# Kernel optimization log

Hardware: AMD Instinct MI355X
Metric: run time of the kernel (lower is better)

Reference implementation:

```python
import jax, jax.numpy as jnp
import numpy as np

N = 16384            # number of input vectors
CODEBOOK_SIZE = 8192  # M
DIM = 256             # dim_feature
BETA = 0.25           # commitment_weight


def setup_inputs() -> dict:
    key = jax.random.key(0)
    kx, ke = jax.random.split(key)
    x = jax.random.normal(kx, (N, DIM), dtype=jnp.float32)
    # kaiming-uniform-style init for the codebook
    bound = float(np.sqrt(3.0 / DIM))
    embeddings = jax.random.uniform(ke, (CODEBOOK_SIZE, DIM), dtype=jnp.float32,
                                    minval=-bound, maxval=bound)
    return {"x": x, "embeddings": embeddings}


def reference(x, embeddings):
    # l2_dist: sqrt(sum((x_i - e_j)^2)) computed via the GEMM expansion
    x2 = jnp.sum(x * x, axis=1, keepdims=True)               # (N, 1)
    e2 = jnp.sum(embeddings * embeddings, axis=1)            # (M,)
    d2 = x2 + e2[None, :] - 2.0 * (x @ embeddings.T)         # (N, M)
    dist = jnp.sqrt(jnp.maximum(d2, 0.0))
    # deterministic gumbel_sample path (training eval / stochastic=False):
    # argmax of logits = -dist  <=>  argmin of dist
    ind = jnp.argmin(dist, axis=1)                           # (N,)
    quantized = embeddings[ind]                              # one_hot @ embeddings
    # commitment loss: beta * ||x_q - sg(x)||^2 (docstring)
    commit_loss = BETA * jnp.mean((quantized - jax.lax.stop_gradient(x)) ** 2)
    # straight-through estimator
    quantized_st = x + jax.lax.stop_gradient(quantized - x)
    # perplexity from per-code counts (one-hot scatter)
    counts = jnp.zeros((CODEBOOK_SIZE,), jnp.float32).at[ind].add(1.0)
    probs = counts / counts.sum()
    perplexity = jnp.exp(-jnp.sum(probs * jnp.log(probs + 1e-10)))
    return quantized_st, ind, commit_loss, perplexity
```

## Files before the change

### kernel.cpp

```cpp
#include <hip/hip_runtime.h>
#include <stdint.h>


#define N_VEC 16384
#define M_CODES 8192
#define DIM 256
#define BETA 0.25f

#define NSLICE 8
#define SLICE_CODES 1024
#define BM 128
#define BN 128
#define BK 32
#define NPART 16
#define LDS_HALF 32768

typedef __attribute__((ext_vector_type(4))) float f32x4;
typedef __attribute__((ext_vector_type(8))) __bf16 bf16x8;

__device__ __forceinline__ void gll16(const void* g, const void* lds) {
    __builtin_amdgcn_global_load_lds(
        (const __attribute__((address_space(1))) uint32_t*)(uintptr_t)g,
        (__attribute__((address_space(3))) uint32_t*)(uint32_t)(uintptr_t)lds,
        16, 0, 0);
}

#define PIPE_SYNC() do { \
    asm volatile("s_waitcnt vmcnt(0)" ::: "memory"); \
    asm volatile("s_barrier" ::: "memory"); \
} while (0)

__device__ __forceinline__ ushort f2bf(float f) {
    uint32_t u = __float_as_uint(f);
    return (ushort)((u + 0x7FFFu + ((u >> 16) & 1u)) >> 16);
}
__device__ __forceinline__ float bf2f(ushort h) {
    return __uint_as_float(((uint32_t)h) << 16);
}

__global__ __launch_bounds__(256) void prep_kernel(
    const float* __restrict__ x, const float* __restrict__ emb,
    ushort* __restrict__ xh, ushort* __restrict__ xl,
    ushort* __restrict__ eh, ushort* __restrict__ el,
    float* __restrict__ e2) {
    const int wave = threadIdx.x >> 6;
    const int lane = threadIdx.x & 63;
    const int row = blockIdx.x * 4 + wave;

    const float* src;
    ushort* ph;
    ushort* pl;
    bool is_e;
    int er = row - N_VEC;
    if (row < N_VEC) {
        src = x + (size_t)row * DIM;
        ph = xh + (size_t)row * DIM;
        pl = xl + (size_t)row * DIM;
        is_e = false;
    } else {
        src = emb + (size_t)er * DIM;
        ph = eh + (size_t)er * DIM;
        pl = el + (size_t)er * DIM;
        is_e = true;
    }
    float4 v = *(const float4*)(src + lane * 4);
    ushort h0 = f2bf(v.x), h1 = f2bf(v.y), h2 = f2bf(v.z), h3 = f2bf(v.w);
    ushort l0 = f2bf(v.x - bf2f(h0)), l1 = f2bf(v.y - bf2f(h1));
    ushort l2 = f2bf(v.z - bf2f(h2)), l3 = f2bf(v.w - bf2f(h3));
    *(ushort4*)(ph + lane * 4) = make_ushort4(h0, h1, h2, h3);
    *(ushort4*)(pl + lane * 4) = make_ushort4(l0, l1, l2, l3);
    if (is_e) {
        float s = v.x * v.x + v.y * v.y + v.z * v.z + v.w * v.w;
        #pragma unroll
        for (int off = 32; off; off >>= 1) s += __shfl_xor(s, off);
        if (lane == 0) e2[er] = s;
    }
}

__global__ __launch_bounds__(256, 2) void vq_mfma_kernel(
    const ushort* __restrict__ xh, const ushort* __restrict__ xl,
    const ushort* __restrict__ eh, const ushort* __restrict__ el,
    const float* __restrict__ e2g, unsigned long long* __restrict__ partials) {
    extern __shared__ char lds[];

    const int t = threadIdx.x;
    const int lane = t & 63;
    const int wv = t >> 6;
    const int lane15 = lane & 15;
    const int l16 = lane >> 4;

    const int bid = blockIdx.x;
    const int rt = bid & 127;
    const int slice = bid >> 7;
    const int row0 = rt * BM;
    const int cslice0 = slice * SLICE_CODES;

    const int wr0 = (wv & 1) * 64;
    const int wc0 = (wv >> 1) * 64;

    int byteA[4], byteB[4];
    #pragma unroll
    for (int f = 0; f < 4; ++f) {
        int ra = wr0 + f * 16 + lane15;
        byteA[f] = ra * 64 + (((l16 ^ (ra >> 1)) & 3) << 4);
        int rb = wc0 + f * 16 + lane15;
        byteB[f] = rb * 64 + (((l16 ^ (rb >> 1)) & 3) << 4);
    }

    const int s0 = wv * 128 + lane;
    const int s1 = s0 + 64;
    const int r0s = s0 >> 2, r1s = s1 >> 2;
    const int c0s = ((s0 & 3) ^ ((s0 >> 3) & 3)) << 3;
    const int c1s = ((s1 & 3) ^ ((s1 >> 3) & 3)) << 3;
    const ushort* pxh0 = xh + (size_t)(row0 + r0s) * DIM + c0s;
    const ushort* pxh1 = xh + (size_t)(row0 + r1s) * DIM + c1s;
    const ushort* pxl0 = xl + (size_t)(row0 + r0s) * DIM + c0s;
    const ushort* pxl1 = xl + (size_t)(row0 + r1s) * DIM + c1s;
    const ushort* peh0 = eh + (size_t)(cslice0 + r0s) * DIM + c0s;
    const ushort* peh1 = eh + (size_t)(cslice0 + r1s) * DIM + c1s;
    const ushort* pel0 = el + (size_t)(cslice0 + r0s) * DIM + c0s;
    const ushort* pel1 = el + (size_t)(cslice0 + r1s) * DIM + c1s;

    float best[16];
    int bidx[16];
    #pragma unroll
    for (int s = 0; s < 16; ++s) { best[s] = __uint_as_float(0x7f800000u); bidx[s] = 0; }

    f32x4 acc[4][4];
    #pragma unroll
    for (int fi = 0; fi < 4; ++fi)
        #pragma unroll
        for (int fj = 0; fj < 4; ++fj) acc[fi][fj] = (f32x4){0.f, 0.f, 0.f, 0.f};

    auto stage = [&](int buf, int ks) {
        const int ct = ks >> 3;
        const int kc = ks & 7;
        const size_t xo = (size_t)(kc << 5);
        const size_t eo = (size_t)ct * ((size_t)BN * DIM) + (kc << 5);
        char* l0 = lds + buf * LDS_HALF + wv * 2048;
        char* l1 = l0 + 1024;
        gll16(pxh0 + xo, l0);
        gll16(pxh1 + xo, l1);
        gll16(pxl0 + xo, l0 + 8192);
        gll16(pxl1 + xo, l1 + 8192);
        gll16(peh0 + eo, l0 + 16384);
        gll16(peh1 + eo, l1 + 16384);
        gll16(pel0 + eo, l0 + 24576);
        gll16(pel1 + eo, l1 + 24576);
    };

    stage(0, 0);
    PIPE_SYNC();

    int cur = 0;
    for (int ks = 0; ks < 64; ++ks) {
        if (ks < 63) stage(cur ^ 1, ks + 1);

        const char* lb = lds + cur * LDS_HALF;
        bf16x8 ah[4], bh[4];
        #pragma unroll
        for (int f = 0; f < 4; ++f) {
            ah[f] = *(const bf16x8*)(lb + byteA[f]);
            bh[f] = *(const bf16x8*)(lb + 16384 + byteB[f]);
        }
        #pragma unroll
        for (int fi = 0; fi < 4; ++fi)
            #pragma unroll
            for (int fj = 0; fj < 4; ++fj)
                acc[fi][fj] = __builtin_amdgcn_mfma_f32_16x16x32_bf16(
                    ah[fi], bh[fj], acc[fi][fj], 0, 0, 0);
        bf16x8 blo[4];
        #pragma unroll
        for (int f = 0; f < 4; ++f) blo[f] = *(const bf16x8*)(lb + 24576 + byteB[f]);
        #pragma unroll
        for (int fi = 0; fi < 4; ++fi)
            #pragma unroll
            for (int fj = 0; fj < 4; ++fj)
                acc[fi][fj] = __builtin_amdgcn_mfma_f32_16x16x32_bf16(
                    ah[fi], blo[fj], acc[fi][fj], 0, 0, 0);
        bf16x8 alo[4];
        #pragma unroll
        for (int f = 0; f < 4; ++f) alo[f] = *(const bf16x8*)(lb + 8192 + byteA[f]);
        #pragma unroll
        for (int fi = 0; fi < 4; ++fi)
            #pragma unroll
            for (int fj = 0; fj < 4; ++fj)
                acc[fi][fj] = __builtin_amdgcn_mfma_f32_16x16x32_bf16(
                    alo[fi], bh[fj], acc[fi][fj], 0, 0, 0);

        PIPE_SYNC();
        cur ^= 1;

        if ((ks & 7) == 7) {
            const int cb = cslice0 + (ks >> 3) * BN + wc0;
            #pragma unroll
            for (int fj = 0; fj < 4; ++fj) {
                const int c = cb + fj * 16 + lane15;
                const float e2v = e2g[c];
                #pragma unroll
                for (int fi = 0; fi < 4; ++fi)
                    #pragma unroll
                    for (int r = 0; r < 4; ++r) {
                        float sc = e2v - 2.0f * acc[fi][fj][r];
                        const int slot = fi * 4 + r;
                        if (sc < best[slot]) { best[slot] = sc; bidx[slot] = c; }
                    }
            }
            #pragma unroll
            for (int fi = 0; fi < 4; ++fi)
                #pragma unroll
                for (int fj = 0; fj < 4; ++fj) acc[fi][fj] = (f32x4){0.f, 0.f, 0.f, 0.f};
        }
    }

    #pragma unroll
    for (int slot = 0; slot < 16; ++slot) {
        float v = best[slot];
        int ix = bidx[slot];
        #pragma unroll
        for (int off = 1; off < 16; off <<= 1) {
            float v2 = __shfl_xor(v, off);
            int ix2 = __shfl_xor(ix, off);
            if (v2 < v || (v2 == v && ix2 < ix)) { v = v2; ix = ix2; }
        }
        if (lane15 == 0) {
            int fi = slot >> 2, r = slot & 3;
            int row = row0 + wr0 + fi * 16 + l16 * 4 + r;
            uint32_t u = __float_as_uint(v);
            uint32_t ord = (u & 0x80000000u) ? ~u : (u | 0x80000000u);
            partials[(size_t)(slice * 2 + (wv >> 1)) * N_VEC + row] =
                ((unsigned long long)ord << 32) | (unsigned)ix;
        }
    }
}

__global__ __launch_bounds__(256) void finish_kernel(
    const float* __restrict__ x, const float* __restrict__ emb,
    const unsigned long long* __restrict__ partials,
    float* __restrict__ out_ind, float* __restrict__ out_q,
    unsigned* __restrict__ counts, float* __restrict__ loss_acc) {
    __shared__ float partial[4];
    const int wave = threadIdx.x >> 6;
    const int lane = threadIdx.x & 63;
    const int row = blockIdx.x * 4 + wave;

    unsigned long long m = ~0ull;
    if (lane < NPART) m = partials[(size_t)lane * N_VEC + row];
    #pragma unroll
    for (int off = 1; off < NPART; off <<= 1) {
        unsigned long long v = __shfl_xor(m, off);
        if (v < m) m = v;
    }
    m = __shfl(m, 0);
    const int ix = (int)(unsigned)(m & 0xFFFFFFFFull);

    float4 q = *(const float4*)(emb + (size_t)ix * DIM + lane * 4);
    float4 xv = *(const float4*)(x + (size_t)row * DIM + lane * 4);
    *(float4*)(out_q + (size_t)row * DIM + lane * 4) = q;
    float dx = q.x - xv.x, dy = q.y - xv.y, dz = q.z - xv.z, dw = q.w - xv.w;
    float s = dx * dx + dy * dy + dz * dz + dw * dw;
    #pragma unroll
    for (int off = 32; off; off >>= 1) s += __shfl_xor(s, off);
    if (lane == 0) {
        out_ind[row] = (float)ix;
        atomicAdd(&counts[ix], 1u);
        partial[wave] = s;
    }
    __syncthreads();
    if (threadIdx.x == 0)
        atomicAdd(loss_acc, partial[0] + partial[1] + partial[2] + partial[3]);
}

__global__ __launch_bounds__(256) void finalize_kernel(
    const unsigned* __restrict__ counts, const float* __restrict__ loss_acc,
    float* __restrict__ out_scalars) {
    __shared__ float red[256];
    float h = 0.0f;
    for (int c = threadIdx.x; c < M_CODES; c += 256) {
        float p = (float)counts[c] * (1.0f / (float)N_VEC);
        h += p * logf(p + 1e-10f);
    }
    red[threadIdx.x] = h;
    __syncthreads();
    for (int s = 128; s; s >>= 1) {
        if (threadIdx.x < s) red[threadIdx.x] += red[threadIdx.x + s];
        __syncthreads();
    }
    if (threadIdx.x == 0) {
        out_scalars[0] = BETA * loss_acc[0] / (float)(N_VEC * DIM);
        out_scalars[1] = expf(-red[0]);
    }
}

extern "C" void kernel_launch(void* const* d_in, const int* in_sizes, int n_in,
                              void* d_out, int out_size, void* d_ws, size_t ws_size,
                              hipStream_t stream) {
    const float* x = (const float*)d_in[0];
    const float* emb = (const float*)d_in[1];

    float* out = (float*)d_out;
    float* out_q = out;
    float* out_ind = out + (size_t)N_VEC * DIM;
    float* out_scalars = out_ind + N_VEC;

    ushort* xh = (ushort*)out;
    ushort* xl = xh + (size_t)N_VEC * DIM;

    char* wp = (char*)d_ws;
    ushort* eh = (ushort*)wp;  wp += (size_t)M_CODES * DIM * 2;
    ushort* el = (ushort*)wp;  wp += (size_t)M_CODES * DIM * 2;
    float* e2 = (float*)wp;    wp += (size_t)M_CODES * 4;
    unsigned long long* partials = (unsigned long long*)wp;
    wp += (size_t)NPART * N_VEC * 8;
    unsigned* counts = (unsigned*)wp; wp += (size_t)M_CODES * 4;
    float* loss_acc = (float*)wp;

    hipMemsetAsync(counts, 0, M_CODES * 4, stream);
    hipMemsetAsync(loss_acc, 0, 4, stream);

    prep_kernel<<<(N_VEC + M_CODES) / 4, 256, 0, stream>>>(x, emb, xh, xl, eh, el, e2);

    hipFuncSetAttribute((const void*)vq_mfma_kernel,
                        hipFuncAttributeMaxDynamicSharedMemorySize, 2 * LDS_HALF);
    vq_mfma_kernel<<<128 * NSLICE, 256, 2 * LDS_HALF, stream>>>(xh, xl, eh, el, e2,
                                                                partials);

    finish_kernel<<<N_VEC / 4, 256, 0, stream>>>(x, emb, partials, out_ind, out_q,
                                                 counts, loss_acc);
    finalize_kernel<<<1, 256, 0, stream>>>(counts, loss_acc, out_scalars);
}
```

Measured before the change: 277.2 us.

## Use 256-row tiles with 512 threads and a three-stage global-to-LDS ring

Doubles the row tile to 256 per block, run by 8 waves, so each staged codebook tile is shared by more rows. The double buffer with a full vmcnt(0) wait becomes a three-slot LDS ring that prefetches two steps ahead and waits only on the oldest step's loads. It also caches the slice's e2 values in LDS, raises wave priority around the MFMA bursts, reorders block indices so the slice varies fastest, and moves the counts/loss zeroing into prep_kernel to drop the memsets. The roughly 148 KB of LDS per block limits each CU to one block, and the larger tile adds register pressure.

```diff
diff --git a/kernel.cpp b/kernel.cpp
--- a/kernel.cpp
+++ b/kernel.cpp
@@ -9,26 +9,24 @@
 
 #define NSLICE 8
 #define SLICE_CODES 1024
-#define BM 128
+#define BM 256
 #define BN 128
 #define BK 32
 #define NPART 16
-#define LDS_HALF 32768
+#define STEP_BYTES 49152
+#define RING_BYTES (3 * STEP_BYTES)
+#define LDS_TOTAL (RING_BYTES + 4096)
+#define NSTEPS 64
 
 typedef __attribute__((ext_vector_type(4))) float f32x4;
 typedef __attribute__((ext_vector_type(8))) __bf16 bf16x8;
 
-__device__ __forceinline__ void gll16(const void* g, const void* lds) {
+__device__ __forceinline__ void gll16(const void* g, const void* lds_p) {
     __builtin_amdgcn_global_load_lds(
         (const __attribute__((address_space(1))) uint32_t*)(uintptr_t)g,
-        (__attribute__((address_space(3))) uint32_t*)(uint32_t)(uintptr_t)lds,
+        (__attribute__((address_space(3))) uint32_t*)(uint32_t)(uintptr_t)lds_p,
         16, 0, 0);
 }
-
-#define PIPE_SYNC() do { \
-    asm volatile("s_waitcnt vmcnt(0)" ::: "memory"); \
-    asm volatile("s_barrier" ::: "memory"); \
-} while (0)
 
 __device__ __forceinline__ ushort f2bf(float f) {
     uint32_t u = __float_as_uint(f);
@@ -42,7 +40,13 @@
     const float* __restrict__ x, const float* __restrict__ emb,
     ushort* __restrict__ xh, ushort* __restrict__ xl,
     ushort* __restrict__ eh, ushort* __restrict__ el,
-    float* __restrict__ e2) {
+    float* __restrict__ e2, unsigned* __restrict__ counts,
+    float* __restrict__ loss_acc) {
+    if (blockIdx.x < 8) {
+        int4 z = {0, 0, 0, 0};
+        ((int4*)counts)[blockIdx.x * 256 + threadIdx.x] = z;
+        if (blockIdx.x == 0 && threadIdx.x == 0) *loss_acc = 0.0f;
+    }
     const int wave = threadIdx.x >> 6;
     const int lane = threadIdx.x & 63;
     const int row = blockIdx.x * 4 + wave;
@@ -77,7 +81,7 @@
     }
 }
 
-__global__ __launch_bounds__(256, 2) void vq_mfma_kernel(
+__global__ __launch_bounds__(512, 2) void vq_mfma_kernel(
     const ushort* __restrict__ xh, const ushort* __restrict__ xl,
     const ushort* __restrict__ eh, const ushort* __restrict__ el,
     const float* __restrict__ e2g, unsigned long long* __restrict__ partials) {
@@ -89,14 +93,13 @@
     const int lane15 = lane & 15;
     const int l16 = lane >> 4;
 
-    const int bid = blockIdx.x;
-    const int rt = bid & 127;
-    const int slice = bid >> 7;
+    const int slice = blockIdx.x & 7;
+    const int rt = blockIdx.x >> 3;
     const int row0 = rt * BM;
     const int cslice0 = slice * SLICE_CODES;
 
-    const int wr0 = (wv & 1) * 64;
-    const int wc0 = (wv >> 1) * 64;
+    const int wr0 = (wv & 3) * 64;
+    const int wc0 = (wv >> 2) * 64;
 
     int byteA[4], byteB[4];
     #pragma unroll
@@ -107,19 +110,19 @@
         byteB[f] = rb * 64 + (((l16 ^ (rb >> 1)) & 3) << 4);
     }
 
-    const int s0 = wv * 128 + lane;
-    const int s1 = s0 + 64;
-    const int r0s = s0 >> 2, r1s = s1 >> 2;
-    const int c0s = ((s0 & 3) ^ ((s0 >> 3) & 3)) << 3;
-    const int c1s = ((s1 & 3) ^ ((s1 >> 3) & 3)) << 3;
-    const ushort* pxh0 = xh + (size_t)(row0 + r0s) * DIM + c0s;
-    const ushort* pxh1 = xh + (size_t)(row0 + r1s) * DIM + c1s;
-    const ushort* pxl0 = xl + (size_t)(row0 + r0s) * DIM + c0s;
-    const ushort* pxl1 = xl + (size_t)(row0 + r1s) * DIM + c1s;
-    const ushort* peh0 = eh + (size_t)(cslice0 + r0s) * DIM + c0s;
-    const ushort* peh1 = eh + (size_t)(cslice0 + r1s) * DIM + c1s;
-    const ushort* pel0 = el + (size_t)(cslice0 + r0s) * DIM + c0s;
-    const ushort* pel1 = el + (size_t)(cslice0 + r1s) * DIM + c1s;
+    const int r_a = t >> 2;
+    const int c_a = ((t & 3) ^ ((t >> 3) & 3));
+    const ushort* pxh_a = xh + (size_t)(row0 + r_a) * DIM + c_a * 8;
+    const ushort* pxh_b = pxh_a + (size_t)128 * DIM;
+    const ushort* pxl_a = xl + (size_t)(row0 + r_a) * DIM + c_a * 8;
+    const ushort* pxl_b = pxl_a + (size_t)128 * DIM;
+    const ushort* peh = eh + (size_t)(cslice0 + r_a) * DIM + c_a * 8;
+    const ushort* pel = el + (size_t)(cslice0 + r_a) * DIM + c_a * 8;
+
+    float* e2s = (float*)(lds + RING_BYTES);
+    e2s[t] = e2g[cslice0 + t];
+    e2s[t + 512] = e2g[cslice0 + t + 512];
+    asm volatile("s_waitcnt lgkmcnt(0)" ::: "memory");
 
     float best[16];
     int bidx[16];
@@ -132,71 +135,59 @@
         #pragma unroll
         for (int fj = 0; fj < 4; ++fj) acc[fi][fj] = (f32x4){0.f, 0.f, 0.f, 0.f};
 
-    auto stage = [&](int buf, int ks) {
-        const int ct = ks >> 3;
-        const int kc = ks & 7;
-        const size_t xo = (size_t)(kc << 5);
-        const size_t eo = (size_t)ct * ((size_t)BN * DIM) + (kc << 5);
-        char* l0 = lds + buf * LDS_HALF + wv * 2048;
-        char* l1 = l0 + 1024;
-        gll16(pxh0 + xo, l0);
-        gll16(pxh1 + xo, l1);
-        gll16(pxl0 + xo, l0 + 8192);
-        gll16(pxl1 + xo, l1 + 8192);
-        gll16(peh0 + eo, l0 + 16384);
-        gll16(peh1 + eo, l1 + 16384);
-        gll16(pel0 + eo, l0 + 24576);
-        gll16(pel1 + eo, l1 + 24576);
+    auto stage = [&](int sidx) {
+        const int ct = sidx >> 3;
+        const int kc = sidx & 7;
+        char* base = lds + (sidx % 3) * STEP_BYTES + wv * 1024;
+        const int xo = kc * 32;
+        const size_t eo = ((size_t)ct << 15) + xo;
+        gll16(pxh_a + xo, base);
+        gll16(pxh_b + xo, base + 8192);
+        gll16(pxl_a + xo, base + 16384);
+        gll16(pxl_b + xo, base + 24576);
+        gll16(peh + eo, base + 32768);
+        gll16(pel + eo, base + 40960);
     };
 
-    stage(0, 0);
-    PIPE_SYNC();
-
-    int cur = 0;
-    for (int ks = 0; ks < 64; ++ks) {
-        if (ks < 63) stage(cur ^ 1, ks + 1);
-
-        const char* lb = lds + cur * LDS_HALF;
-        bf16x8 ah[4], bh[4];
+    auto compute = [&](int sidx) {
+        const char* lb = lds + (sidx % 3) * STEP_BYTES;
+        bf16x8 ah[4], alo[4], bh[4], blo[4];
         #pragma unroll
         for (int f = 0; f < 4; ++f) {
             ah[f] = *(const bf16x8*)(lb + byteA[f]);
-            bh[f] = *(const bf16x8*)(lb + 16384 + byteB[f]);
+            alo[f] = *(const bf16x8*)(lb + 16384 + byteA[f]);
+            bh[f] = *(const bf16x8*)(lb + 32768 + byteB[f]);
+            blo[f] = *(const bf16x8*)(lb + 40960 + byteB[f]);
         }
+        __builtin_amdgcn_s_setprio(1);
         #pragma unroll
         for (int fi = 0; fi < 4; ++fi)
             #pragma unroll
             for (int fj = 0; fj < 4; ++fj)
                 acc[fi][fj] = __builtin_amdgcn_mfma_f32_16x16x32_bf16(
                     ah[fi], bh[fj], acc[fi][fj], 0, 0, 0);
-        bf16x8 blo[4];
-        #pragma unroll
-        for (int f = 0; f < 4; ++f) blo[f] = *(const bf16x8*)(lb + 24576 + byteB[f]);
         #pragma unroll
         for (int fi = 0; fi < 4; ++fi)
             #pragma unroll
             for (int fj = 0; fj < 4; ++fj)
                 acc[fi][fj] = __builtin_amdgcn_mfma_f32_16x16x32_bf16(
                     ah[fi], blo[fj], acc[fi][fj], 0, 0, 0);
-        bf16x8 alo[4];
-        #pragma unroll
-        for (int f = 0; f < 4; ++f) alo[f] = *(const bf16x8*)(lb + 8192 + byteA[f]);
         #pragma unroll
         for (int fi = 0; fi < 4; ++fi)
             #pragma unroll
             for (int fj = 0; fj < 4; ++fj)
                 acc[fi][fj] = __builtin_amdgcn_mfma_f32_16x16x32_bf16(
                     alo[fi], bh[fj], acc[fi][fj], 0, 0, 0);
-
-        PIPE_SYNC();
-        cur ^= 1;
-
-        if ((ks & 7) == 7) {
-            const int cb = cslice0 + (ks >> 3) * BN + wc0;
+        __builtin_amdgcn_s_setprio(0);
+
+        if ((sidx & 7) == 7) {
+            const int ct = sidx >> 3;
+            const int cb = cslice0 + ct * BN + wc0;
             #pragma unroll
             for (int fj = 0; fj < 4; ++fj) {
+                const int cl = ct * BN + wc0 + fj * 16 + lane15;
+                const float e2v = e2s[cl];
                 const int c = cb + fj * 16 + lane15;
-                const float e2v = e2g[c];
                 #pragma unroll
                 for (int fi = 0; fi < 4; ++fi)
                     #pragma unroll
@@ -211,7 +202,20 @@
                 #pragma unroll
                 for (int fj = 0; fj < 4; ++fj) acc[fi][fj] = (f32x4){0.f, 0.f, 0.f, 0.f};
         }
-    }
+    };
+
+    stage(0);
+    stage(1);
+
+    for (int sidx = 0; sidx < NSTEPS - 1; ++sidx) {
+        asm volatile("s_waitcnt vmcnt(6)" ::: "memory");
+        __builtin_amdgcn_s_barrier();
+        if (sidx < NSTEPS - 2) stage(sidx + 2);
+        compute(sidx);
+    }
+    asm volatile("s_waitcnt vmcnt(0)" ::: "memory");
+    __builtin_amdgcn_s_barrier();
+    compute(NSTEPS - 1);
 
     #pragma unroll
     for (int slot = 0; slot < 16; ++slot) {
@@ -228,7 +232,7 @@
             int row = row0 + wr0 + fi * 16 + l16 * 4 + r;
             uint32_t u = __float_as_uint(v);
             uint32_t ord = (u & 0x80000000u) ? ~u : (u | 0x80000000u);
-            partials[(size_t)(slice * 2 + (wv >> 1)) * N_VEC + row] =
+            partials[(size_t)(slice * 2 + (wv >> 2)) * N_VEC + row] =
                 ((unsigned long long)ord << 32) | (unsigned)ix;
         }
     }
@@ -315,15 +319,13 @@
     unsigned* counts = (unsigned*)wp; wp += (size_t)M_CODES * 4;
     float* loss_acc = (float*)wp;
 
-    hipMemsetAsync(counts, 0, M_CODES * 4, stream);
-    hipMemsetAsync(loss_acc, 0, 4, stream);
-
-    prep_kernel<<<(N_VEC + M_CODES) / 4, 256, 0, stream>>>(x, emb, xh, xl, eh, el, e2);
+    prep_kernel<<<(N_VEC + M_CODES) / 4, 256, 0, stream>>>(x, emb, xh, xl, eh, el,
+                                                           e2, counts, loss_acc);
 
     hipFuncSetAttribute((const void*)vq_mfma_kernel,
-                        hipFuncAttributeMaxDynamicSharedMemorySize, 2 * LDS_HALF);
-    vq_mfma_kernel<<<128 * NSLICE, 256, 2 * LDS_HALF, stream>>>(xh, xl, eh, el, e2,
-                                                                partials);
+                        hipFuncAttributeMaxDynamicSharedMemorySize, LDS_TOTAL);
+    vq_mfma_kernel<<<(N_VEC / BM) * NSLICE, 512, LDS_TOTAL, stream>>>(
+        xh, xl, eh, el, e2, partials);
 
     finish_kernel<<<N_VEC / 4, 256, 0, stream>>>(x, emb, partials, out_ind, out_q,
                                                  counts, loss_acc);
```

Result: faster. 271.6 us (-2.0%).
